# Kernel optimization log

Hardware: AMD Instinct MI355X
Metric: run time of the kernel (lower is better)

The kernel has to match this reference:

```python
import jax, jax.numpy as jnp
import numpy as np

T, B, N = 512, 256, 128


def setup_inputs() -> dict:
    key = jax.random.key(0)
    k1, k2, k3, k4, k5, k6 = jax.random.split(key, 6)
    emit = jax.random.normal(k1, (T, B, N), dtype=jnp.float32)
    target = jax.random.randint(k2, (T, B), 0, N)
    # prefix-true mask from random lengths in [1, T]
    lengths = jax.random.randint(k3, (B,), 1, T + 1)
    mask = jnp.arange(T)[:, None] < lengths[None, :]
    std = (1.0 / N) ** 0.5
    trans = jax.random.normal(k4, (N, N), dtype=jnp.float32) * std
    strans = jax.random.normal(k5, (N,), dtype=jnp.float32) * std
    etrans = jax.random.normal(k6, (N,), dtype=jnp.float32) * std
    return {"emit": emit, "target": target, "mask": mask,
            "trans": trans, "strans": strans, "etrans": etrans}


def _logZ(emit, mask, trans, strans, etrans):
    alpha0 = strans + emit[0]  # (B, N)

    def step(alpha, xs):
        e_t, m_t = xs  # (B, N), (B,)
        # scores[b, j] = logsumexp_i(alpha[b, i] + trans[i, j] + e_t[b, j])
        scores = jax.scipy.special.logsumexp(
            alpha[:, :, None] + trans[None, :, :] + e_t[:, None, :], axis=1)
        alpha = jnp.where(m_t[:, None], scores, alpha)
        return alpha, None

    alpha, _ = jax.lax.scan(step, alpha0, (emit[1:], mask[1:]))
    return jax.scipy.special.logsumexp(alpha + etrans, axis=1).sum()


def _score(emit, target, mask, trans, strans, etrans):
    Tn, Bn, _ = emit.shape
    # emission scores of gold tags: (T, B)
    sc = jnp.take_along_axis(emit, target[:, :, None], axis=2)[..., 0]
    # transition scores between consecutive gold tags
    sc = sc.at[1:].add(trans[target[:-1], target[1:]])
    score = jnp.sum(jnp.where(mask, sc, jnp.float32(0.0)))
    ends = mask.astype(jnp.int32).sum(axis=0) - 1  # (B,)
    score = score + strans[target[0]].sum()
    score = score + etrans[target[ends, jnp.arange(Bn)]].sum()
    return score


def reference(emit, target, mask, trans, strans, etrans):
    Bn = emit.shape[1]
    logZ = _logZ(emit, mask, trans, strans, etrans)
    score = _score(emit, target, mask, trans, strans, etrans)
    return (logZ - score) / Bn
```

## Files before the change

### kernel.cpp

```cpp
#include <hip/hip_runtime.h>

#define TT 512
#define BB 256
#define NN 128
#define MW 16
#define NWG (BB / MW)
#define STH 144

#define LENS_OFF 256
#define AF_OFF 2048
#define CF_OFF (AF_OFF + BB * NN * 4)
#define BU_OFF (CF_OFF + 1024)
#define CB_OFF (BU_OFF + BB * NN * 4)
#define XQ_OFF (CB_OFF + 1024)
#define XQ_SZ ((size_t)TT * BB * NN * 2)

typedef __attribute__((ext_vector_type(8))) short short8_t;
typedef __attribute__((ext_vector_type(4))) float f32x4;

__device__ __forceinline__ unsigned short f2bf(float f) {
  unsigned u = __float_as_uint(f);
  return (unsigned short)((u + 0x7FFF + ((u >> 16) & 1)) >> 16);
}
__device__ __forceinline__ float bf2f(unsigned short h) {
  return __uint_as_float(((unsigned)h) << 16);
}
__device__ __forceinline__ int orig_j(int p) {
  return 32 * (p >> 5) + 16 * (p & 1) + ((p >> 1) & 15);
}

__global__ __launch_bounds__(256) void crf_expemit(
    const float* __restrict__ emit, uint4* __restrict__ Xq) {
  const int bid = blockIdx.x;
  const int g = bid >> 9;
  const int t = bid & (TT - 1);
  const int tid = threadIdx.x;
  const int w = tid >> 6, l = tid & 63, qd = l >> 4, c = l & 15;
  const int bg = g * MW;
  unsigned pk[4];
#pragma unroll
  for (int r = 0; r < 4; ++r) {
    const size_t row = ((size_t)t * BB + bg + 4 * qd + r) * NN + 32 * w + c;
    float v0 = __expf(emit[row]);
    float v1 = __expf(emit[row + 16]);
    pk[r] = (unsigned)f2bf(v0) | ((unsigned)f2bf(v1) << 16);
  }
  Xq[((size_t)g * TT + t) * 256 + tid] = make_uint4(pk[0], pk[1], pk[2], pk[3]);
}

__global__ __launch_bounds__(BB) void crf_score_k(
    const float* __restrict__ emit, const int* __restrict__ target,
    const void* __restrict__ maskp, const float* __restrict__ trans,
    const float* __restrict__ strans, const float* __restrict__ etrans,
    float* __restrict__ ws, int* __restrict__ lens) {
  __shared__ float rf[4];
  const int b = threadIdx.x;
  const int t = blockIdx.x;
  const unsigned char* mk8 = (const unsigned char*)maskp;
  const int* mk32 = (const int*)maskp;
  const bool is_u8 = (mk8[1] != 0);

  int m = is_u8 ? (mk8[t * BB + b] != 0) : (mk32[t * BB + b] != 0);
  float v = 0.f;
  if (m) {
    int tg = target[t * BB + b];
    v = emit[((size_t)t * BB + b) * NN + tg];
    v += (t > 0) ? trans[target[(t - 1) * BB + b] * NN + tg] : strans[tg];
    int mn = (t + 1 < TT) ? (is_u8 ? (mk8[(t + 1) * BB + b] != 0)
                                   : (mk32[(t + 1) * BB + b] != 0))
                          : 0;
    if (!mn) {
      v += etrans[tg];
      lens[b] = t + 1;
    }
  }
#pragma unroll
  for (int off = 32; off; off >>= 1) v += __shfl_down(v, off, 64);
  if ((b & 63) == 0) rf[b >> 6] = v;
  __syncthreads();
  if (b == 0) atomicAdd(&ws[1], rf[0] + rf[1] + rf[2] + rf[3]);
}

__global__ __launch_bounds__(256, 1) void crf_fb(
    const float* __restrict__ emit, const float* __restrict__ trans,
    const float* __restrict__ strans, const float* __restrict__ etrans,
    const uint4* __restrict__ Xq, const int* __restrict__ lens,
    float* __restrict__ AF, int* __restrict__ CF,
    float* __restrict__ BU, int* __restrict__ CB) {
  __shared__ __align__(16) unsigned short sV[2][MW * STH];
  __shared__ __align__(16) int nrm[2][MW];
  __shared__ __align__(16) int sC[MW];
  __shared__ int slen[MW];
  __shared__ int smax_s;

  const int tid = threadIdx.x;
  const int w = tid >> 6;
  const int l = tid & 63;
  const int c = l & 15;
  const int qd = l >> 4;
  const bool bwd = (blockIdx.x >= NWG);
  const int g = bwd ? (int)blockIdx.x - NWG : (int)blockIdx.x;
  const int bg = g * MW;

  if (tid == 0) smax_s = 0;
  if (tid < MW) slen[tid] = lens[bg + tid];
  __syncthreads();
  if (tid < MW) atomicMax(&smax_s, slen[tid]);

  short8_t eB[4][2];
#pragma unroll
  for (int kt = 0; kt < 4; ++kt)
#pragma unroll
    for (int u = 0; u < 2; ++u)
#pragma unroll
      for (int jj = 0; jj < 8; ++jj) {
        int kp = kt * 32 + qd * 8 + jj;
        int a_ = orig_j(kp);
        int b_ = 32 * w + 16 * u + c;
        float tv = bwd ? trans[b_ * NN + a_] : trans[a_ * NN + b_];
        eB[kt][u][jj] = (short)f2bf(__expf(tv));
      }
  const float eet0 = __expf(etrans[32 * w + c]);
  const float eet1 = __expf(etrans[32 * w + 16 + c]);

  {
    const int m = tid & 15;
    const int pbase = (tid >> 4) * 8;
    if (!bwd) {
      const int b = bg + m;
#pragma unroll
      for (int pp = 0; pp < 8; ++pp) {
        int p = pbase + pp;
        int j = orig_j(p);
        float v = __expf(strans[j] + emit[(size_t)b * NN + j]);
        sV[0][m * STH + p] = f2bf(v);
        if (p == 0)
          nrm[0][m] = ((int)((__float_as_uint(v) >> 23) & 0xFF)) - 120;
      }
    } else {
#pragma unroll
      for (int pp = 0; pp < 8; ++pp) {
        int p = pbase + pp;
        sV[0][m * STH + p] = 0x3F80;
        sV[1][m * STH + p] = 0x3F80;
        if (p == 0) { nrm[0][m] = 0; nrm[1][m] = 0; }
      }
    }
  }
  __syncthreads();
  const int smax = smax_s;
  int lm1[4];
#pragma unroll
  for (int r = 0; r < 4; ++r) lm1[r] = slen[4 * qd + r] - 1;

  int cloc[4] = {0, 0, 0, 0};
  const bool nwriter = (w == 0 && c == 0);
  const uint4* Xg = Xq + (size_t)g * TT * 256 + tid;

#define FB_MFMA()                                                             \
    const short8_t A0 = *(const short8_t*)&sV[PIN][c * STH + 0 + qd * 8];     \
    const short8_t A1 = *(const short8_t*)&sV[PIN][c * STH + 32 + qd * 8];    \
    const short8_t A2 = *(const short8_t*)&sV[PIN][c * STH + 64 + qd * 8];    \
    const short8_t A3 = *(const short8_t*)&sV[PIN][c * STH + 96 + qd * 8];    \
    const int4 nr = *(const int4*)&nrm[PIN][4 * qd];                          \
    f32x4 p0 = {0.f, 0.f, 0.f, 0.f}, q0 = {0.f, 0.f, 0.f, 0.f};              \
    f32x4 p1 = {0.f, 0.f, 0.f, 0.f}, q1 = {0.f, 0.f, 0.f, 0.f};              \
    p0 = __builtin_amdgcn_mfma_f32_16x16x32_bf16(A0, eB[0][0], p0, 0, 0, 0); \
    p1 = __builtin_amdgcn_mfma_f32_16x16x32_bf16(A0, eB[0][1], p1, 0, 0, 0); \
    q0 = __builtin_amdgcn_mfma_f32_16x16x32_bf16(A2, eB[2][0], q0, 0, 0, 0); \
    q1 = __builtin_amdgcn_mfma_f32_16x16x32_bf16(A2, eB[2][1], q1, 0, 0, 0); \
    p0 = __builtin_amdgcn_mfma_f32_16x16x32_bf16(A1, eB[1][0], p0, 0, 0, 0); \
    p1 = __builtin_amdgcn_mfma_f32_16x16x32_bf16(A1, eB[1][1], p1, 0, 0, 0); \
    q0 = __builtin_amdgcn_mfma_f32_16x16x32_bf16(A3, eB[3][0], q0, 0, 0, 0); \
    q1 = __builtin_amdgcn_mfma_f32_16x16x32_bf16(A3, eB[3][1], q1, 0, 0, 0); \
    const f32x4 ac0 = p0 + q0;                                                \
    const f32x4 ac1 = p1 + q1;                                                \
    const int nA[4] = {nr.x, nr.y, nr.z, nr.w};

  if (!bwd) {
    const int LmaxF = (smax < 258) ? smax : 258;
    for (int tb = 1; tb < LmaxF; tb += 8) {
      uint4 xq[8];
#pragma unroll
      for (int k = 0; k < 8; ++k) {
        int t = tb + k;
        if (t > TT - 1) t = TT - 1;
        xq[k] = Xg[(size_t)t * 256];
      }
#pragma unroll
      for (int k = 0; k < 8; ++k) {
        const int T_ = tb + k;
        if (T_ >= LmaxF) break;
        const int POUT = T_ & 1, PIN = POUT ^ 1;
        FB_MFMA();
        const unsigned xd[4] = {xq[k].x, xq[k].y, xq[k].z, xq[k].w};
        int nnw[4];
#pragma unroll
        for (int r_ = 0; r_ < 4; ++r_) {
          float x0 = __uint_as_float(xd[r_] << 16);
          float x1 = __uint_as_float(xd[r_] & 0xffff0000u);
          float v0 = ldexpf(ac0[r_] * x0, -nA[r_]);
          float v1 = ldexpf(ac1[r_] * x1, -nA[r_]);
          if (T_ <= lm1[r_]) {
            unsigned pk = (unsigned)f2bf(v0) | ((unsigned)f2bf(v1) << 16);
            *(unsigned*)&sV[POUT][(4 * qd + r_) * STH + 32 * w + 2 * c] = pk;
            cloc[r_] += nA[r_];
          }
          nnw[r_] = ((int)((__float_as_uint(v0) >> 23) & 0xFF)) - 120;
        }
        if (nwriter)
          *(int4*)&nrm[POUT][4 * qd] = make_int4(nnw[0], nnw[1], nnw[2], nnw[3]);
        __syncthreads();
      }
    }
  } else if (smax >= 259) {
    for (int tb = smax - 1; tb >= 258; tb -= 8) {
      uint4 xq[8];
#pragma unroll
      for (int k = 0; k < 8; ++k) {
        int t = tb - k;
        if (t < 258) t = 258;
        xq[k] = Xg[(size_t)t * 256];
      }
#pragma unroll
      for (int k = 0; k < 8; ++k) {
        const int T_ = tb - k;
        if (T_ < 258) break;
        const int POUT = T_ & 1, PIN = POUT ^ 1;
        FB_MFMA();
        const unsigned xd[4] = {xq[k].x, xq[k].y, xq[k].z, xq[k].w};
        int nnw[4];
#pragma unroll
        for (int r_ = 0; r_ < 4; ++r_) {
          float x0 = __uint_as_float(xd[r_] << 16);
          float x1 = __uint_as_float(xd[r_] & 0xffff0000u);
          const bool isact = (T_ == lm1[r_]);
          float v0 = isact ? x0 * eet0 : ldexpf(ac0[r_] * x0, -nA[r_]);
          float v1 = isact ? x1 * eet1 : ldexpf(ac1[r_] * x1, -nA[r_]);
          if (T_ <= lm1[r_]) {
            unsigned pk = (unsigned)f2bf(v0) | ((unsigned)f2bf(v1) << 16);
            *(unsigned*)&sV[POUT][(4 * qd + r_) * STH + 32 * w + 2 * c] = pk;
            cloc[r_] = isact ? 0 : cloc[r_] + nA[r_];
          }
          nnw[r_] = ((int)((__float_as_uint(v0) >> 23) & 0xFF)) - 120;
        }
        if (nwriter)
          *(int4*)&nrm[POUT][4 * qd] = make_int4(nnw[0], nnw[1], nnw[2], nnw[3]);
        __syncthreads();
      }
    }
  }
#undef FB_MFMA

  if (nwriter)
    *(int4*)&sC[4 * qd] = make_int4(cloc[0], cloc[1], cloc[2], cloc[3]);
  __syncthreads();
  {
    const int m = tid >> 4, i16 = tid & 15;
    if (!bwd) {
      int nf = slen[m] - 1;
      if (nf > 257) nf = 257;
      const int pf = nf & 1;
#pragma unroll
      for (int pp = 0; pp < 8; ++pp) {
        int p = i16 * 8 + pp;
        AF[(size_t)(bg + m) * NN + p] = bf2f(sV[pf][m * STH + p]);
      }
      if (i16 == 0) CF[bg + m] = sC[m];
    } else {
#pragma unroll
      for (int pp = 0; pp < 8; ++pp) {
        int p = i16 * 8 + pp;
        BU[(size_t)(bg + m) * NN + p] = bf2f(sV[0][m * STH + p]);
      }
      if (i16 == 0) CB[bg + m] = sC[m];
    }
  }
}

__global__ __launch_bounds__(256) void crf_comb(
    const float* __restrict__ trans, const float* __restrict__ etrans,
    const int* __restrict__ lens, const float* __restrict__ AF,
    const int* __restrict__ CF, const float* __restrict__ BU,
    const int* __restrict__ CB, float* __restrict__ ws,
    float* __restrict__ out) {
  __shared__ __align__(16) unsigned short sU[MW * STH];
  __shared__ float sRed[4][MW][2];
  __shared__ int slen[MW];
  const int tid = threadIdx.x;
  const int w = tid >> 6, l = tid & 63, c = l & 15, qd = l >> 4;
  const int g = blockIdx.x, bg = g * MW;

  if (tid < MW) slen[tid] = lens[bg + tid];
  {
    const int m = tid & 15, pbase = (tid >> 4) * 8;
#pragma unroll
    for (int pp = 0; pp < 8; ++pp) {
      int p = pbase + pp;
      sU[m * STH + p] = f2bf(BU[(size_t)(bg + m) * NN + p]);
    }
  }
  short8_t eB[4][2];
#pragma unroll
  for (int kt = 0; kt < 4; ++kt)
#pragma unroll
    for (int u = 0; u < 2; ++u)
#pragma unroll
      for (int jj = 0; jj < 8; ++jj) {
        int kp = kt * 32 + qd * 8 + jj;
        int a_ = orig_j(kp);
        int b_ = 32 * w + 16 * u + c;
        eB[kt][u][jj] = (short)f2bf(__expf(trans[b_ * NN + a_]));
      }
  const float eet0 = __expf(etrans[32 * w + c]);
  const float eet1 = __expf(etrans[32 * w + 16 + c]);
  __syncthreads();

  const short8_t A0 = *(const short8_t*)&sU[c * STH + 0 + qd * 8];
  const short8_t A1 = *(const short8_t*)&sU[c * STH + 32 + qd * 8];
  const short8_t A2 = *(const short8_t*)&sU[c * STH + 64 + qd * 8];
  const short8_t A3 = *(const short8_t*)&sU[c * STH + 96 + qd * 8];
  f32x4 ac0 = {0.f, 0.f, 0.f, 0.f}, ac1 = {0.f, 0.f, 0.f, 0.f};
  ac0 = __builtin_amdgcn_mfma_f32_16x16x32_bf16(A0, eB[0][0], ac0, 0, 0, 0);
  ac1 = __builtin_amdgcn_mfma_f32_16x16x32_bf16(A0, eB[0][1], ac1, 0, 0, 0);
  ac0 = __builtin_amdgcn_mfma_f32_16x16x32_bf16(A1, eB[1][0], ac0, 0, 0, 0);
  ac1 = __builtin_amdgcn_mfma_f32_16x16x32_bf16(A1, eB[1][1], ac1, 0, 0, 0);
  ac0 = __builtin_amdgcn_mfma_f32_16x16x32_bf16(A2, eB[2][0], ac0, 0, 0, 0);
  ac1 = __builtin_amdgcn_mfma_f32_16x16x32_bf16(A2, eB[2][1], ac1, 0, 0, 0);
  ac0 = __builtin_amdgcn_mfma_f32_16x16x32_bf16(A3, eB[3][0], ac0, 0, 0, 0);
  ac1 = __builtin_amdgcn_mfma_f32_16x16x32_bf16(A3, eB[3][1], ac1, 0, 0, 0);

#pragma unroll
  for (int r_ = 0; r_ < 4; ++r_) {
    float a0 = AF[(size_t)(bg + 4 * qd + r_) * NN + 32 * w + 2 * c];
    float a1 = AF[(size_t)(bg + 4 * qd + r_) * NN + 32 * w + 2 * c + 1];
    float dB = a0 * ac0[r_] + a1 * ac1[r_];
    float dA = a0 * eet0 + a1 * eet1;
#pragma unroll
    for (int mk = 1; mk < 16; mk <<= 1) {
      dB += __shfl_xor(dB, mk, 64);
      dA += __shfl_xor(dA, mk, 64);
    }
    if (c == 0) {
      sRed[w][4 * qd + r_][0] = dB;
      sRed[w][4 * qd + r_][1] = dA;
    }
  }
  __syncthreads();
  if (tid < MW) {
    float DB = sRed[0][tid][0] + sRed[1][tid][0] + sRed[2][tid][0] + sRed[3][tid][0];
    float DA = sRed[0][tid][1] + sRed[1][tid][1] + sRed[2][tid][1] + sRed[3][tid][1];
    const int len = slen[tid];
    const float LN2 = 0.6931471805599453f;
    float logZ;
    if (len >= 259)
      logZ = LN2 * (float)(CF[bg + tid] + CB[bg + tid]) + __logf(DB);
    else
      logZ = LN2 * (float)CF[bg + tid] + __logf(DA);
    atomicAdd(&ws[0], logZ);
  }
  __syncthreads();
  if (tid == 0) {
    __threadfence();
    unsigned old = atomicAdd((unsigned*)ws + 3, 1u);
    if (old == NWG - 1) {
      float zz = atomicAdd(&ws[0], 0.f);
      float ss = atomicAdd(&ws[1], 0.f);
      out[0] = (zz - ss) * (1.0f / (float)BB);
    }
  }
}

__global__ __launch_bounds__(256, 1) void crf_fused_fb(
    const float* __restrict__ emit, const int* __restrict__ target,
    const void* __restrict__ maskp, const float* __restrict__ trans,
    const float* __restrict__ strans, const float* __restrict__ etrans,
    float* __restrict__ ws, float* __restrict__ out) {
  __shared__ __align__(16) unsigned short sV[2][MW * STH];
  __shared__ __align__(16) int nrm[2][MW];
  __shared__ __align__(16) int sC[MW];
  __shared__ int slen[MW];
  __shared__ float sscore;
  __shared__ int smax;

  const int tid = threadIdx.x;
  const int w = tid >> 6;
  const int l = tid & 63;
  const int c = l & 15;
  const int qd = l >> 4;
  const int bg = blockIdx.x * MW;

  if (tid < MW) slen[tid] = 0;
  if (tid == 0) { sscore = 0.f; smax = 0; }
  __syncthreads();

  const unsigned char* mk8 = (const unsigned char*)maskp;
  const int* mk32 = (const int*)maskp;
  const bool is_u8 = (mk8[1] != 0);
  {
    const int mi = tid & 15;
    const int b = bg + mi;
    const int t0 = (tid >> 4) * 32;
    int cnt = 0;
    float sc = 0.f;
    for (int s = 0; s < 32; ++s) {
      int t = t0 + s;
      int m = is_u8 ? (mk8[t * BB + b] != 0) : (mk32[t * BB + b] != 0);
      if (m) {
        cnt++;
        int tg = target[t * BB + b];
        float v = emit[((size_t)t * BB + b) * NN + tg];
        v += (t > 0) ? trans[target[(t - 1) * BB + b] * NN + tg] : strans[tg];
        int mn = (t + 1 < TT) ? (is_u8 ? (mk8[(t + 1) * BB + b] != 0)
                                       : (mk32[(t + 1) * BB + b] != 0))
                              : 0;
        if (!mn) v += etrans[tg];
        sc += v;
      }
    }
    atomicAdd(&slen[mi], cnt);
    atomicAdd(&sscore, sc);
  }

  short8_t eB[4][2];
#pragma unroll
  for (int kt = 0; kt < 4; ++kt)
#pragma unroll
    for (int u = 0; u < 2; ++u)
#pragma unroll
      for (int jj = 0; jj < 8; ++jj) {
        int kp = kt * 32 + qd * 8 + jj;
        int i = orig_j(kp);
        int j = 32 * w + 16 * u + c;
        eB[kt][u][jj] = (short)f2bf(__expf(trans[i * NN + j]));
      }

  {
    const int m = tid & 15;
    const int b = bg + m;
    const int pbase = (tid >> 4) * 8;
#pragma unroll
    for (int pp = 0; pp < 8; ++pp) {
      int p = pbase + pp;
      int j = orig_j(p);
      float v = __expf(strans[j] + emit[(size_t)b * NN + j]);
      sV[0][m * STH + p] = f2bf(v);
      if (p == 0)
        nrm[0][m] = ((int)((__float_as_uint(v) >> 23) & 0xFF)) - 120;
    }
  }
  __syncthreads();

  if (tid < MW) atomicMax(&smax, slen[tid]);
  if (tid == 0) atomicAdd(&ws[1], sscore);
  __syncthreads();
  const int Lmax = smax;
  int lenr[4];
#pragma unroll
  for (int r = 0; r < 4; ++r) lenr[r] = slen[4 * qd + r];

  int off8[8];
#pragma unroll
  for (int r = 0; r < 4; ++r)
#pragma unroll
    for (int u = 0; u < 2; ++u)
      off8[r * 2 + u] = (bg + 4 * qd + r) * NN + 32 * w + 16 * u + c;

  float ra[8], rb[8], xv[8];
  {
#pragma unroll
    for (int i = 0; i < 8; ++i) ra[i] = emit[(size_t)1 * BB * NN + off8[i]];
#pragma unroll
    for (int i = 0; i < 8; ++i) rb[i] = emit[(size_t)2 * BB * NN + off8[i]];
#pragma unroll
    for (int i = 0; i < 8; ++i) xv[i] = __expf(ra[i]);
  }
  int cloc[4] = {0, 0, 0, 0};
  const bool nwriter = (w == 0 && c == 0);

#define CRF_STEP(T_, PIN, POUT, RL, RO)                                       \
  do {                                                                        \
    int tl = ((T_) + 2 < TT) ? (T_) + 2 : TT - 1;                             \
    const size_t gbase = (size_t)tl * (BB * NN);                              \
    _Pragma("unroll") for (int i_ = 0; i_ < 8; ++i_)                          \
        RL[i_] = emit[gbase + off8[i_]];                                      \
    const short8_t A0 = *(const short8_t*)&sV[PIN][c * STH + 0 + qd * 8];     \
    const short8_t A1 = *(const short8_t*)&sV[PIN][c * STH + 32 + qd * 8];    \
    const short8_t A2 = *(const short8_t*)&sV[PIN][c * STH + 64 + qd * 8];    \
    const short8_t A3 = *(const short8_t*)&sV[PIN][c * STH + 96 + qd * 8];    \
    const int4 nr = *(const int4*)&nrm[PIN][4 * qd];                          \
    f32x4 ac0 = {0.f, 0.f, 0.f, 0.f}, ac1 = {0.f, 0.f, 0.f, 0.f};             \
    ac0 = __builtin_amdgcn_mfma_f32_16x16x32_bf16(A0, eB[0][0], ac0, 0, 0, 0);\
    ac1 = __builtin_amdgcn_mfma_f32_16x16x32_bf16(A0, eB[0][1], ac1, 0, 0, 0);\
    ac0 = __builtin_amdgcn_mfma_f32_16x16x32_bf16(A1, eB[1][0], ac0, 0, 0, 0);\
    ac1 = __builtin_amdgcn_mfma_f32_16x16x32_bf16(A1, eB[1][1], ac1, 0, 0, 0);\
    ac0 = __builtin_amdgcn_mfma_f32_16x16x32_bf16(A2, eB[2][0], ac0, 0, 0, 0);\
    ac1 = __builtin_amdgcn_mfma_f32_16x16x32_bf16(A2, eB[2][1], ac1, 0, 0, 0);\
    ac0 = __builtin_amdgcn_mfma_f32_16x16x32_bf16(A3, eB[3][0], ac0, 0, 0, 0);\
    ac1 = __builtin_amdgcn_mfma_f32_16x16x32_bf16(A3, eB[3][1], ac1, 0, 0, 0);\
    const int nA[4] = {nr.x, nr.y, nr.z, nr.w};                               \
    int nnw[4];                                                               \
    _Pragma("unroll") for (int r_ = 0; r_ < 4; ++r_) {                        \
      float y0 = ac0[r_] * xv[2 * r_];                                        \
      float y1 = ac1[r_] * xv[2 * r_ + 1];                                    \
      float v0 = ldexpf(y0, -nA[r_]);                                         \
      float v1 = ldexpf(y1, -nA[r_]);                                         \
      if ((T_) < lenr[r_]) {                                                  \
        unsigned pk = (unsigned)f2bf(v0) | ((unsigned)f2bf(v1) << 16);        \
        *(unsigned*)&sV[POUT][(4 * qd + r_) * STH + 32 * w + 2 * c] = pk;     \
        cloc[r_] += nA[r_];                                                   \
      }                                                                       \
      nnw[r_] = ((int)((__float_as_uint(v0) >> 23) & 0xFF)) - 120;            \
    }                                                                         \
    if (nwriter)                                                              \
      *(int4*)&nrm[POUT][4 * qd] = make_int4(nnw[0], nnw[1], nnw[2], nnw[3]); \
    _Pragma("unroll") for (int i_ = 0; i_ < 8; ++i_)                          \
        xv[i_] = __expf(RO[i_]);                                              \
    __syncthreads();                                                          \
  } while (0)

  for (int t = 1; t < Lmax; t += 2) {
    CRF_STEP(t, 0, 1, ra, rb);
    if (t + 1 < Lmax) {
      CRF_STEP(t + 1, 1, 0, rb, ra);
    }
  }
#undef CRF_STEP

  if (nwriter) *(int4*)&sC[4 * qd] = make_int4(cloc[0], cloc[1], cloc[2], cloc[3]);
  __syncthreads();
  {
    const int m = tid >> 4, i16 = tid & 15;
    const int pb = (slen[m] - 1) & 1;
    float s = 0.f;
#pragma unroll
    for (int pp = 0; pp < 8; ++pp) {
      int p = i16 * 8 + pp;
      int j = orig_j(p);
      s += bf2f(sV[pb][m * STH + p]) * __expf(etrans[j]);
    }
    s += __shfl_xor(s, 1, 64);
    s += __shfl_xor(s, 2, 64);
    s += __shfl_xor(s, 4, 64);
    s += __shfl_xor(s, 8, 64);
    if (i16 == 0)
      atomicAdd(&ws[0], (float)sC[m] * 0.69314718f + __logf(s));
  }
  __syncthreads();
  if (tid == 0) {
    __threadfence();
    unsigned old = atomicAdd((unsigned*)ws + 3, 1u);
    if (old == NWG - 1) {
      float zz = atomicAdd(&ws[0], 0.f);
      float ss = atomicAdd(&ws[1], 0.f);
      out[0] = (zz - ss) * (1.0f / (float)BB);
    }
  }
}

extern "C" void kernel_launch(void* const* d_in, const int* in_sizes, int n_in,
                              void* d_out, int out_size, void* d_ws, size_t ws_size,
                              hipStream_t stream) {
  const float* emit = (const float*)d_in[0];
  const int* target = (const int*)d_in[1];
  const void* mask = (const void*)d_in[2];
  const float* trans = (const float*)d_in[3];
  const float* strans = (const float*)d_in[4];
  const float* etrans = (const float*)d_in[5];
  float* ws = (float*)d_ws;
  float* out = (float*)d_out;

  const size_t need = (size_t)XQ_OFF + XQ_SZ;
  hipMemsetAsync(d_ws, 0, 16, stream);
  if (ws_size >= need) {
    int* lens = (int*)((char*)d_ws + LENS_OFF);
    float* AF = (float*)((char*)d_ws + AF_OFF);
    int* CF = (int*)((char*)d_ws + CF_OFF);
    float* BU = (float*)((char*)d_ws + BU_OFF);
    int* CB = (int*)((char*)d_ws + CB_OFF);
    uint4* Xq = (uint4*)((char*)d_ws + XQ_OFF);
    crf_expemit<<<NWG * TT, 256, 0, stream>>>(emit, Xq);
    crf_score_k<<<TT, BB, 0, stream>>>(emit, target, mask, trans, strans,
                                       etrans, ws, lens);
    crf_fb<<<2 * NWG, 256, 0, stream>>>(emit, trans, strans, etrans,
                                        (const uint4*)Xq, lens, AF, CF, BU, CB);
    crf_comb<<<NWG, 256, 0, stream>>>(trans, etrans, lens, AF, CF, BU, CB, ws,
                                      out);
  } else {
    crf_fused_fb<<<NWG, 256, 0, stream>>>(emit, target, mask, trans, strans,
                                          etrans, ws, out);
  }
}
```

Baseline: 260.0 us.

## Fuse preprocessing kernels, renormalize every other step, use packed bf16 convert

Merges the exp-emission packing kernel and the gold-path score kernel into one launch, removing one kernel launch and its serialization. In the recurrent forward/backward loop, the per-step exponent renormalization (ldexpf and the shared-memory norm exchange) now runs only on odd steps, with a separate double-buffered norm array. Even steps do a plain multiply. bf16 packing uses the hardware v_cvt_pk_bf16_f32 instruction, and the barrier becomes a raw s_waitcnt plus s_barrier. Skipping every other renormalization risks bf16 overflow or underflow range drift, and the hand-written barrier relies on the compiler not reordering LDS accesses around it.

```diff
diff --git a/kernel.cpp b/kernel.cpp
--- a/kernel.cpp
+++ b/kernel.cpp
@@ -28,60 +28,68 @@
 __device__ __forceinline__ int orig_j(int p) {
   return 32 * (p >> 5) + 16 * (p & 1) + ((p >> 1) & 15);
 }
-
-__global__ __launch_bounds__(256) void crf_expemit(
-    const float* __restrict__ emit, uint4* __restrict__ Xq) {
-  const int bid = blockIdx.x;
-  const int g = bid >> 9;
-  const int t = bid & (TT - 1);
-  const int tid = threadIdx.x;
-  const int w = tid >> 6, l = tid & 63, qd = l >> 4, c = l & 15;
-  const int bg = g * MW;
-  unsigned pk[4];
-#pragma unroll
-  for (int r = 0; r < 4; ++r) {
-    const size_t row = ((size_t)t * BB + bg + 4 * qd + r) * NN + 32 * w + c;
-    float v0 = __expf(emit[row]);
-    float v1 = __expf(emit[row + 16]);
-    pk[r] = (unsigned)f2bf(v0) | ((unsigned)f2bf(v1) << 16);
-  }
-  Xq[((size_t)g * TT + t) * 256 + tid] = make_uint4(pk[0], pk[1], pk[2], pk[3]);
-}
-
-__global__ __launch_bounds__(BB) void crf_score_k(
+__device__ __forceinline__ unsigned pk_bf16(float a, float b) {
+  unsigned r;
+  asm("v_cvt_pk_bf16_f32 %0, %1, %2" : "=v"(r) : "v"(a), "v"(b));
+  return r;
+}
+
+#define BARRIER_LGKM() \
+  asm volatile("s_waitcnt lgkmcnt(0)\n\ts_barrier" ::: "memory")
+
+__global__ __launch_bounds__(256) void crf_pre(
     const float* __restrict__ emit, const int* __restrict__ target,
     const void* __restrict__ maskp, const float* __restrict__ trans,
     const float* __restrict__ strans, const float* __restrict__ etrans,
-    float* __restrict__ ws, int* __restrict__ lens) {
+    uint4* __restrict__ Xq, float* __restrict__ ws, int* __restrict__ lens) {
   __shared__ float rf[4];
-  const int b = threadIdx.x;
-  const int t = blockIdx.x;
-  const unsigned char* mk8 = (const unsigned char*)maskp;
-  const int* mk32 = (const int*)maskp;
-  const bool is_u8 = (mk8[1] != 0);
-
-  int m = is_u8 ? (mk8[t * BB + b] != 0) : (mk32[t * BB + b] != 0);
-  float v = 0.f;
-  if (m) {
-    int tg = target[t * BB + b];
-    v = emit[((size_t)t * BB + b) * NN + tg];
-    v += (t > 0) ? trans[target[(t - 1) * BB + b] * NN + tg] : strans[tg];
-    int mn = (t + 1 < TT) ? (is_u8 ? (mk8[(t + 1) * BB + b] != 0)
-                                   : (mk32[(t + 1) * BB + b] != 0))
-                          : 0;
-    if (!mn) {
-      v += etrans[tg];
-      lens[b] = t + 1;
-    }
-  }
-#pragma unroll
-  for (int off = 32; off; off >>= 1) v += __shfl_down(v, off, 64);
-  if ((b & 63) == 0) rf[b >> 6] = v;
-  __syncthreads();
-  if (b == 0) atomicAdd(&ws[1], rf[0] + rf[1] + rf[2] + rf[3]);
-}
-
-__global__ __launch_bounds__(256, 1) void crf_fb(
+  const int bid = blockIdx.x;
+  if (bid < NWG * TT) {
+    const int g = bid >> 9;
+    const int t = bid & (TT - 1);
+    const int tid = threadIdx.x;
+    const int w = tid >> 6, l = tid & 63, qd = l >> 4, c = l & 15;
+    const int bg = g * MW;
+    unsigned pk[4];
+#pragma unroll
+    for (int r = 0; r < 4; ++r) {
+      const size_t row = ((size_t)t * BB + bg + 4 * qd + r) * NN + 32 * w + c;
+      float v0 = __expf(emit[row]);
+      float v1 = __expf(emit[row + 16]);
+      pk[r] = (unsigned)f2bf(v0) | ((unsigned)f2bf(v1) << 16);
+    }
+    Xq[((size_t)g * TT + t) * 256 + tid] =
+        make_uint4(pk[0], pk[1], pk[2], pk[3]);
+  } else {
+    const int b = threadIdx.x;
+    const int t = bid - NWG * TT;
+    const unsigned char* mk8 = (const unsigned char*)maskp;
+    const int* mk32 = (const int*)maskp;
+    const bool is_u8 = (mk8[1] != 0);
+
+    int m = is_u8 ? (mk8[t * BB + b] != 0) : (mk32[t * BB + b] != 0);
+    float v = 0.f;
+    if (m) {
+      int tg = target[t * BB + b];
+      v = emit[((size_t)t * BB + b) * NN + tg];
+      v += (t > 0) ? trans[target[(t - 1) * BB + b] * NN + tg] : strans[tg];
+      int mn = (t + 1 < TT) ? (is_u8 ? (mk8[(t + 1) * BB + b] != 0)
+                                     : (mk32[(t + 1) * BB + b] != 0))
+                            : 0;
+      if (!mn) {
+        v += etrans[tg];
+        lens[b] = t + 1;
+      }
+    }
+#pragma unroll
+    for (int off = 32; off; off >>= 1) v += __shfl_down(v, off, 64);
+    if ((b & 63) == 0) rf[b >> 6] = v;
+    __syncthreads();
+    if (b == 0) atomicAdd(&ws[1], rf[0] + rf[1] + rf[2] + rf[3]);
+  }
+}
+
+__global__ __launch_bounds__(256, 1) void crf_fb3(
     const float* __restrict__ emit, const float* __restrict__ trans,
     const float* __restrict__ strans, const float* __restrict__ etrans,
     const uint4* __restrict__ Xq, const int* __restrict__ lens,
@@ -154,6 +162,7 @@
   for (int r = 0; r < 4; ++r) lm1[r] = slen[4 * qd + r] - 1;
 
   int cloc[4] = {0, 0, 0, 0};
+  int nb = 0;
   const bool nwriter = (w == 0 && c == 0);
   const uint4* Xg = Xq + (size_t)g * TT * 256 + tid;
 
@@ -162,7 +171,6 @@
     const short8_t A1 = *(const short8_t*)&sV[PIN][c * STH + 32 + qd * 8];    \
     const short8_t A2 = *(const short8_t*)&sV[PIN][c * STH + 64 + qd * 8];    \
     const short8_t A3 = *(const short8_t*)&sV[PIN][c * STH + 96 + qd * 8];    \
-    const int4 nr = *(const int4*)&nrm[PIN][4 * qd];                          \
     f32x4 p0 = {0.f, 0.f, 0.f, 0.f}, q0 = {0.f, 0.f, 0.f, 0.f};              \
     f32x4 p1 = {0.f, 0.f, 0.f, 0.f}, q1 = {0.f, 0.f, 0.f, 0.f};              \
     p0 = __builtin_amdgcn_mfma_f32_16x16x32_bf16(A0, eB[0][0], p0, 0, 0, 0); \
@@ -174,8 +182,7 @@
     q0 = __builtin_amdgcn_mfma_f32_16x16x32_bf16(A3, eB[3][0], q0, 0, 0, 0); \
     q1 = __builtin_amdgcn_mfma_f32_16x16x32_bf16(A3, eB[3][1], q1, 0, 0, 0); \
     const f32x4 ac0 = p0 + q0;                                                \
-    const f32x4 ac1 = p1 + q1;                                                \
-    const int nA[4] = {nr.x, nr.y, nr.z, nr.w};
+    const f32x4 ac1 = p1 + q1;
 
   if (!bwd) {
     const int LmaxF = (smax < 258) ? smax : 258;
@@ -192,25 +199,44 @@
         const int T_ = tb + k;
         if (T_ >= LmaxF) break;
         const int POUT = T_ & 1, PIN = POUT ^ 1;
+        const bool NORM = (k & 1) != 0;
         FB_MFMA();
         const unsigned xd[4] = {xq[k].x, xq[k].y, xq[k].z, xq[k].w};
-        int nnw[4];
-#pragma unroll
-        for (int r_ = 0; r_ < 4; ++r_) {
-          float x0 = __uint_as_float(xd[r_] << 16);
-          float x1 = __uint_as_float(xd[r_] & 0xffff0000u);
-          float v0 = ldexpf(ac0[r_] * x0, -nA[r_]);
-          float v1 = ldexpf(ac1[r_] * x1, -nA[r_]);
-          if (T_ <= lm1[r_]) {
-            unsigned pk = (unsigned)f2bf(v0) | ((unsigned)f2bf(v1) << 16);
-            *(unsigned*)&sV[POUT][(4 * qd + r_) * STH + 32 * w + 2 * c] = pk;
-            cloc[r_] += nA[r_];
+        if (NORM) {
+          const int4 nr = *(const int4*)&nrm[nb][4 * qd];
+          const int nA[4] = {nr.x, nr.y, nr.z, nr.w};
+          int nnw[4];
+#pragma unroll
+          for (int r_ = 0; r_ < 4; ++r_) {
+            float x0 = __uint_as_float(xd[r_] << 16);
+            float x1 = __uint_as_float(xd[r_] & 0xffff0000u);
+            float v0 = ldexpf(ac0[r_] * x0, -nA[r_]);
+            float v1 = ldexpf(ac1[r_] * x1, -nA[r_]);
+            if (T_ <= lm1[r_]) {
+              *(unsigned*)&sV[POUT][(4 * qd + r_) * STH + 32 * w + 2 * c] =
+                  pk_bf16(v0, v1);
+              cloc[r_] += nA[r_];
+            }
+            nnw[r_] = ((int)((__float_as_uint(v0) >> 23) & 0xFF)) - 120;
           }
-          nnw[r_] = ((int)((__float_as_uint(v0) >> 23) & 0xFF)) - 120;
+          if (nwriter)
+            *(int4*)&nrm[nb ^ 1][4 * qd] =
+                make_int4(nnw[0], nnw[1], nnw[2], nnw[3]);
+          nb ^= 1;
+        } else {
+#pragma unroll
+          for (int r_ = 0; r_ < 4; ++r_) {
+            float x0 = __uint_as_float(xd[r_] << 16);
+            float x1 = __uint_as_float(xd[r_] & 0xffff0000u);
+            float v0 = ac0[r_] * x0;
+            float v1 = ac1[r_] * x1;
+            if (T_ <= lm1[r_]) {
+              *(unsigned*)&sV[POUT][(4 * qd + r_) * STH + 32 * w + 2 * c] =
+                  pk_bf16(v0, v1);
+            }
+          }
         }
-        if (nwriter)
-          *(int4*)&nrm[POUT][4 * qd] = make_int4(nnw[0], nnw[1], nnw[2], nnw[3]);
-        __syncthreads();
+        BARRIER_LGKM();
       }
     }
   } else if (smax >= 259) {
@@ -227,26 +253,47 @@
         const int T_ = tb - k;
         if (T_ < 258) break;
         const int POUT = T_ & 1, PIN = POUT ^ 1;
+        const bool NORM = (k & 1) != 0;
         FB_MFMA();
         const unsigned xd[4] = {xq[k].x, xq[k].y, xq[k].z, xq[k].w};
-        int nnw[4];
-#pragma unroll
-        for (int r_ = 0; r_ < 4; ++r_) {
-          float x0 = __uint_as_float(xd[r_] << 16);
-          float x1 = __uint_as_float(xd[r_] & 0xffff0000u);
-          const bool isact = (T_ == lm1[r_]);
-          float v0 = isact ? x0 * eet0 : ldexpf(ac0[r_] * x0, -nA[r_]);
-          float v1 = isact ? x1 * eet1 : ldexpf(ac1[r_] * x1, -nA[r_]);
-          if (T_ <= lm1[r_]) {
-            unsigned pk = (unsigned)f2bf(v0) | ((unsigned)f2bf(v1) << 16);
-            *(unsigned*)&sV[POUT][(4 * qd + r_) * STH + 32 * w + 2 * c] = pk;
-            cloc[r_] = isact ? 0 : cloc[r_] + nA[r_];
+        if (NORM) {
+          const int4 nr = *(const int4*)&nrm[nb][4 * qd];
+          const int nA[4] = {nr.x, nr.y, nr.z, nr.w};
+          int nnw[4];
+#pragma unroll
+          for (int r_ = 0; r_ < 4; ++r_) {
+            float x0 = __uint_as_float(xd[r_] << 16);
+            float x1 = __uint_as_float(xd[r_] & 0xffff0000u);
+            const bool isact = (T_ == lm1[r_]);
+            float v0 = isact ? x0 * eet0 : ldexpf(ac0[r_] * x0, -nA[r_]);
+            float v1 = isact ? x1 * eet1 : ldexpf(ac1[r_] * x1, -nA[r_]);
+            if (T_ <= lm1[r_]) {
+              *(unsigned*)&sV[POUT][(4 * qd + r_) * STH + 32 * w + 2 * c] =
+                  pk_bf16(v0, v1);
+              cloc[r_] = isact ? 0 : cloc[r_] + nA[r_];
+            }
+            nnw[r_] = ((int)((__float_as_uint(v0) >> 23) & 0xFF)) - 120;
           }
-          nnw[r_] = ((int)((__float_as_uint(v0) >> 23) & 0xFF)) - 120;
+          if (nwriter)
+            *(int4*)&nrm[nb ^ 1][4 * qd] =
+                make_int4(nnw[0], nnw[1], nnw[2], nnw[3]);
+          nb ^= 1;
+        } else {
+#pragma unroll
+          for (int r_ = 0; r_ < 4; ++r_) {
+            float x0 = __uint_as_float(xd[r_] << 16);
+            float x1 = __uint_as_float(xd[r_] & 0xffff0000u);
+            const bool isact = (T_ == lm1[r_]);
+            float v0 = isact ? x0 * eet0 : ac0[r_] * x0;
+            float v1 = isact ? x1 * eet1 : ac1[r_] * x1;
+            if (T_ <= lm1[r_]) {
+              *(unsigned*)&sV[POUT][(4 * qd + r_) * STH + 32 * w + 2 * c] =
+                  pk_bf16(v0, v1);
+              cloc[r_] = isact ? 0 : cloc[r_];
+            }
+          }
         }
-        if (nwriter)
-          *(int4*)&nrm[POUT][4 * qd] = make_int4(nnw[0], nnw[1], nnw[2], nnw[3]);
-        __syncthreads();
+        BARRIER_LGKM();
       }
     }
   }
@@ -579,11 +626,11 @@
     float* BU = (float*)((char*)d_ws + BU_OFF);
     int* CB = (int*)((char*)d_ws + CB_OFF);
     uint4* Xq = (uint4*)((char*)d_ws + XQ_OFF);
-    crf_expemit<<<NWG * TT, 256, 0, stream>>>(emit, Xq);
-    crf_score_k<<<TT, BB, 0, stream>>>(emit, target, mask, trans, strans,
-                                       etrans, ws, lens);
-    crf_fb<<<2 * NWG, 256, 0, stream>>>(emit, trans, strans, etrans,
-                                        (const uint4*)Xq, lens, AF, CF, BU, CB);
+    crf_pre<<<NWG * TT + TT, 256, 0, stream>>>(emit, target, mask, trans,
+                                               strans, etrans, Xq, ws, lens);
+    crf_fb3<<<2 * NWG, 256, 0, stream>>>(emit, trans, strans, etrans,
+                                         (const uint4*)Xq, lens, AF, CF, BU,
+                                         CB);
     crf_comb<<<NWG, 256, 0, stream>>>(trans, etrans, lens, AF, CF, BU, CB, ws,
                                       out);
   } else {
```

New measurement: 239.3 us. -7.9%, faster.
